# Optimization experiments

Measured on AMD Instinct MI355X. Metric: run time of the kernel, lower is better.

The kernel has to match this reference:

```python
import jax, jax.numpy as jnp
import numpy as np

B, L, E, H = 4, 4096, 1024, 16
D = E // H
SQRT_D = float(np.sqrt(D))


def _g(x):
    # torch: softplus(x, beta=5) ** 2
    sp = jax.nn.softplus(5.0 * x) / 5.0
    return sp * sp


def setup_inputs() -> dict:
    key = jax.random.key(0)
    ks = jax.random.split(key, 7)
    s = 1.0 / np.sqrt(E)
    x = jax.random.normal(ks[0], (B, L, E), jnp.float32)
    Wq = jax.random.normal(ks[1], (E, E), jnp.float32) * s
    bq = jax.random.normal(ks[2], (E,), jnp.float32) * s
    Wk = jax.random.normal(ks[3], (E, E), jnp.float32) * s
    bk = jax.random.normal(ks[4], (E,), jnp.float32) * s
    Wv = jax.random.normal(ks[5], (E, E), jnp.float32) * s
    bv = jax.random.normal(ks[6], (E,), jnp.float32) * s
    return {"x": x, "Wq": Wq, "bq": bq, "Wk": Wk, "bk": bk, "Wv": Wv, "bv": bv}


def _fast_linear_attn(q, k, v):
    # q,k,v: [B,S,H,D]
    Ls = q.shape[1]
    # RALA-style global-query rescaling of K
    q_global = q.mean(axis=1, keepdims=True) / SQRT_D          # [B,1,H,D]
    logits = jnp.einsum('bihd,blhd->bihl', q_global, k)        # [B,1,H,L]
    alpha = jax.nn.softmax(logits, axis=-1) * Ls               # [B,1,H,L]
    alpha = jnp.transpose(alpha[:, 0], (0, 2, 1))[..., None]   # [B,L,H,1]
    k = k * alpha
    gq, gk = _g(q), _g(k)
    gmq, gmk = _g(-q), _g(-k)
    # symmetric / antisymmetric KV accumulation: state [B,H,D,D]
    gk_v = jnp.einsum('bshd,bshv->bhdv', gk, v)
    gmk_v = jnp.einsum('bshd,bshv->bhdv', gmk, v)
    num = (jnp.einsum('bshd,bhdv->bshv', gq, gk_v)
           + jnp.einsum('bshd,bhdv->bshv', gmq, gmk_v))        # [B,S,H,D]
    den = (jnp.einsum('bshd,bhd->bsh', gq, gk.sum(axis=1))
           + jnp.einsum('bshd,bhd->bsh', gmq, gmk.sum(axis=1)))
    return num / (den[..., None] + 1e-6)


def reference(x, Wq, bq, Wk, bk, Wv, bv):
    q = (x @ Wq + bq).reshape(B, L, H, D)
    k = (x @ Wk + bk).reshape(B, L, H, D)
    v = (x @ Wv + bv).reshape(B, L, H, D)
    out = _fast_linear_attn(q, k, v)  # [B,L,H,D]
    return out.reshape(B, L, E)
```

## Files before the change

### kernel.cpp

```cpp
#include <hip/hip_runtime.h>
#include <hip/hip_bf16.h>
#include <math.h>

#define B_ 4
#define L_ 4096
#define E_ 1024
#define H_ 16
#define D_ 64
#define M_ (B_*L_)

typedef __attribute__((ext_vector_type(8))) short s8;
typedef __attribute__((ext_vector_type(4))) float f4;

__device__ __forceinline__ float gfun(float x) {
  float z = fminf(5.0f * x, 60.0f);
  float sp = 0.2f * __logf(1.0f + __expf(z));
  return sp * sp;
}

__device__ __forceinline__ unsigned short f2bf(float v) {
  __hip_bfloat16 h = __float2bfloat16(v);
  return *reinterpret_cast<unsigned short*>(&h);
}
__device__ __forceinline__ float bf2f(unsigned short u) {
  __hip_bfloat16 h = *reinterpret_cast<__hip_bfloat16*>(&u);
  return __bfloat162float(h);
}

__device__ __forceinline__ void gload16(const void* g, void* l) {
  __builtin_amdgcn_global_load_lds(
      (const __attribute__((address_space(1))) void*)g,
      (__attribute__((address_space(3))) void*)l, 16, 0, 0);
}

__global__ __launch_bounds__(256) void split_x(
    const float* __restrict__ x, unsigned short* __restrict__ Ah,
    float* __restrict__ xsum)
{
  int blk = blockIdx.x, t = threadIdx.x;
  int r0 = blk * 64, b = r0 >> 12;
  int c4 = t * 4;
  float4 cs = {0.f, 0.f, 0.f, 0.f};
  for (int r = 0; r < 64; ++r) {
    int row = r0 + r;
    float4 x4 = *(const float4*)(x + (size_t)row * E_ + c4);
    ushort4 hi, lo;
    unsigned short h;
    h = f2bf(x4.x); hi.x = h; lo.x = f2bf(x4.x - bf2f(h));
    h = f2bf(x4.y); hi.y = h; lo.y = f2bf(x4.y - bf2f(h));
    h = f2bf(x4.z); hi.z = h; lo.z = f2bf(x4.z - bf2f(h));
    h = f2bf(x4.w); hi.w = h; lo.w = f2bf(x4.w - bf2f(h));
    *(ushort4*)&Ah[(size_t)row * 2048 + c4]        = hi;
    *(ushort4*)&Ah[(size_t)row * 2048 + 1024 + c4] = lo;
    cs.x += x4.x; cs.y += x4.y; cs.z += x4.z; cs.w += x4.w;
  }
  atomicAdd(&xsum[b * E_ + c4 + 0], cs.x);
  atomicAdd(&xsum[b * E_ + c4 + 1], cs.y);
  atomicAdd(&xsum[b * E_ + c4 + 2], cs.z);
  atomicAdd(&xsum[b * E_ + c4 + 3], cs.w);
}

__global__ __launch_bounds__(256) void split_wT(
    const float* __restrict__ Wq, const float* __restrict__ Wk,
    const float* __restrict__ Wv, const float* __restrict__ bq,
    const float* __restrict__ xsum,
    unsigned short* __restrict__ Bt, float* __restrict__ qg)
{
  int z = blockIdx.z;
  const float* W = (z == 0) ? Wq : (z == 1) ? Wk : Wv;
  __shared__ float tile[32][33];
  int t = threadIdx.x;
  int tx = t & 31, ty = t >> 5;
  int k0 = blockIdx.x * 32, n0 = blockIdx.y * 32;
  #pragma unroll
  for (int i = 0; i < 4; ++i)
    tile[ty + i*8][tx] = W[(size_t)(k0 + ty + i*8) * 1024 + n0 + tx];
  __syncthreads();
  unsigned short* Bz = Bt + (size_t)z * 2097152;
  #pragma unroll
  for (int i = 0; i < 4; ++i) {
    int n = n0 + ty + i*8, kk = k0 + tx;
    float v = tile[tx][ty + i*8];
    unsigned short h = f2bf(v);
    Bz[(size_t)n * 2048 + kk]        = h;
    Bz[(size_t)n * 2048 + 1024 + kk] = f2bf(v - bf2f(h));
  }
  if (z == 0 && t < 128) {
    int n = t & 31, b = t >> 5;
    float dot = 0.f;
    #pragma unroll
    for (int kk = 0; kk < 32; ++kk)
      dot += xsum[b * E_ + k0 + kk] * tile[kk][n];
    float val = dot * (1.0f / (L_ * 8.0f));
    if (k0 == 0) val += bq[n0 + n] * 0.125f;
    atomicAdd(&qg[b * E_ + n0 + n], val);
  }
}

#define PRIO1() __builtin_amdgcn_s_setprio(1)
#define PRIO0() __builtin_amdgcn_s_setprio(0)
#define BARR() do { asm volatile("" ::: "memory"); \
                    __builtin_amdgcn_s_barrier(); \
                    asm volatile("" ::: "memory"); } while (0)
#define WAITL0() asm volatile("s_waitcnt lgkmcnt(0)" ::: "memory")
#define WAITV(n) asm volatile("s_waitcnt vmcnt(" n ")" ::: "memory")

#define STAGE_A(buf, kofs) do { \
  const unsigned short* g_ = gA + (kofs); \
  char* d_ = dA0 + (buf) * 32768; \
  gload16(g_,          d_); \
  gload16(g_ + 131072, d_ +  8192); \
  gload16(g_ + 262144, d_ + 16384); \
  gload16(g_ + 393216, d_ + 24576); \
} while (0)

#define STAGE_B(buf, kofs) do { \
  const unsigned short* g_ = gB + (kofs); \
  char* d_ = dB0 + (buf) * 32768; \
  gload16(g_,          d_); \
  gload16(g_ + 131072, d_ +  8192); \
  gload16(g_ + 262144, d_ + 16384); \
  gload16(g_ + 393216, d_ + 24576); \
} while (0)

#define LDA(buf, mh) do { \
  const char* p_ = shb + (buf) * 32768 + arow + (mh) * 8192; \
  _Pragma("unroll") \
  for (int ii = 0; ii < 4; ++ii) { \
    aF[ii][0] = *(const s8*)(p_ + ii * 2048 + c0); \
    aF[ii][1] = *(const s8*)(p_ + ii * 2048 + c1); \
  } \
} while (0)

#define LDB(buf, nh) do { \
  const char* p_ = shb + 65536 + (buf) * 32768 + brow + (nh) * 4096; \
  _Pragma("unroll") \
  for (int jj = 0; jj < 2; ++jj) { \
    bF[(nh)*2+jj][0] = *(const s8*)(p_ + jj * 2048 + c0); \
    bF[(nh)*2+jj][1] = *(const s8*)(p_ + jj * 2048 + c1); \
  } \
} while (0)

#define MFMAQ(mh, nh) do { \
  _Pragma("unroll") \
  for (int ii = 0; ii < 4; ++ii) \
    _Pragma("unroll") \
    for (int jj = 0; jj < 2; ++jj) { \
      acc[(mh)*4+ii][(nh)*2+jj] = __builtin_amdgcn_mfma_f32_16x16x32_bf16( \
          aF[ii][0], bF[(nh)*2+jj][0], acc[(mh)*4+ii][(nh)*2+jj], 0, 0, 0); \
      acc[(mh)*4+ii][(nh)*2+jj] = __builtin_amdgcn_mfma_f32_16x16x32_bf16( \
          aF[ii][1], bF[(nh)*2+jj][1], acc[(mh)*4+ii][(nh)*2+jj], 0, 0, 0); \
    } \
} while (0)

#define TILE2(buf, doStage, kB_, kA_, vmN) do { \
   \
  LDA(buf, 0); LDB(buf, 0); LDB(buf, 1); \
  WAITL0(); \
  PRIO1(); MFMAQ(0, 0); MFMAQ(0, 1); PRIO0(); \
   \
  LDA(buf, 1); \
  BARR(); \
  WAITL0(); \
  if (doStage) { STAGE_B(buf, kB_); STAGE_A(buf, kA_); } \
  PRIO1(); MFMAQ(1, 0); MFMAQ(1, 1); PRIO0(); \
  WAITV(vmN); \
  BARR(); \
} while (0)

__global__ __launch_bounds__(512, 2) void qkv_mfma(
    const unsigned short* __restrict__ Ah, const unsigned short* __restrict__ Bt,
    const float* __restrict__ bq, const float* __restrict__ bk,
    const float* __restrict__ bv, const float* __restrict__ qg,
    float* __restrict__ aexp, float* __restrict__ denom,
    float* __restrict__ qo, float* __restrict__ ko, float* __restrict__ vo)
{
  __shared__ unsigned short sh[65536];

  const int t  = threadIdx.x;
  const int li = blockIdx.x;
  const int xc = li & 7;
  const int idx = li >> 3;
  const int z   = idx >> 5;
  const int rem = idx & 31;
  const int bm = (xc * 8 + (rem >> 2)) * 256;
  const int bn = (rem & 3) * 256;

  const float* bias = (z == 0) ? bq : (z == 1) ? bk : bv;
  float* out = (z == 0) ? qo : (z == 1) ? ko : vo;
  const unsigned short* Bz = Bt + (size_t)z * 2097152;

  const int srow = t >> 3;
  const int scol = ((t & 7) ^ (srow & 7)) * 8;
  const unsigned short* gA = Ah + (size_t)(bm + srow) * 2048 + scol;
  const unsigned short* gB = Bz + (size_t)(bn + srow) * 2048 + scol;
  char* const shb = (char*)sh;
  char* const dA0 = shb +         t * 16;
  char* const dB0 = shb + 65536 + t * 16;

  const int lane = t & 63, wid = t >> 6;
  const int wm = wid >> 2, wn = wid & 3;
  const int fr = lane & 15, fq = lane >> 4;
  const int c0 = ((fq)     ^ (fr & 7)) * 16;
  const int c1 = ((fq + 4) ^ (fr & 7)) * 16;
  const int arow = (wm * 128 + fr) * 128;
  const int brow = (wn *  64 + fr) * 128;

  f4 acc[8][4] = {};
  s8 aF[4][2], bF[4][2];

  STAGE_B(0, 0);  STAGE_A(0, 0);
  STAGE_B(1, 64); STAGE_A(1, 64);
  WAITV("8");
  BARR();

  #pragma unroll 1
  for (int it = 0; it < 23; ++it) {
    const int t2 = 2 * it + 2, t3 = 2 * it + 3;
    const int kA2 = (t2 < 16) ? t2 * 64 : t2 * 64 - 1024;
    const int kB2 = (t2 < 32) ? t2 * 64 : t2 * 64 - 2048;
    const int kA3 = (t3 < 16) ? t3 * 64 : t3 * 64 - 1024;
    const int kB3 = (t3 < 32) ? t3 * 64 : t3 * 64 - 2048;
    TILE2(0, true, kB2, kA2, "8");
    TILE2(1, true, kB3, kA3, "8");
  }
  TILE2(0, false, 0, 0, "0");
  TILE2(1, false, 0, 0, "0");

  float bv4[4];
  #pragma unroll
  for (int j = 0; j < 4; ++j) bv4[j] = bias[bn + wn * 64 + j * 16 + fr];
  #pragma unroll
  for (int i = 0; i < 8; ++i) {
    const int mrow = bm + wm * 128 + i * 16 + fq * 4;
    #pragma unroll
    for (int j = 0; j < 4; ++j) {
      const int ncol = bn + wn * 64 + j * 16 + fr;
      #pragma unroll
      for (int r = 0; r < 4; ++r)
        out[(size_t)(mrow + r) * E_ + ncol] = acc[i][j][r] + bv4[j];
    }
  }

  if (z == 1) {
    const int b_ = bm >> 12;
    const int h  = (bn >> 6) + wn;
    const int bh = b_ * 16 + h;
    float qgv[4];
    #pragma unroll
    for (int j = 0; j < 4; ++j) qgv[j] = qg[bh * 64 + j * 16 + fr];
    float partial[8][4];
    #pragma unroll
    for (int i = 0; i < 8; ++i)
      #pragma unroll
      for (int r = 0; r < 4; ++r) {
        float p = 0.f;
        #pragma unroll
        for (int j = 0; j < 4; ++j)
          p += qgv[j] * (acc[i][j][r] + bv4[j]);
        p += __shfl_xor(p, 1);
        p += __shfl_xor(p, 2);
        p += __shfl_xor(p, 4);
        p += __shfl_xor(p, 8);
        partial[i][r] = p;
      }
    if (fr == 0) {
      const int lbase = (bm & 4095) + wm * 128 + fq * 4;
      float s = 0.f;
      #pragma unroll
      for (int i = 0; i < 8; ++i)
        #pragma unroll
        for (int r = 0; r < 4; ++r) {
          float e = __expf(partial[i][r]);
          aexp[(size_t)bh * 4096 + lbase + i * 16 + r] = e;
          s += e;
        }
      atomicAdd(&denom[bh], s);
    }
  }
}

__global__ __launch_bounds__(256) void state_part(
    const float* __restrict__ k, const float* __restrict__ v,
    const float* __restrict__ aexp, const float* __restrict__ denom,
    float* __restrict__ Spart, float* __restrict__ SMpart,
    float* __restrict__ kpart, float* __restrict__ kmpart)
{
  __shared__ unsigned short lds[24576];
  const int bh = blockIdx.x, b = bh >> 4, h = bh & 15;
  const int c = blockIdx.y;
  const float scale = (float)L_ / denom[bh];
  const int t = threadIdx.x;

  const int wid = t >> 6, lane = t & 63;
  const int s = wid >> 1, dh = wid & 1;
  const int fr = lane & 15, fq = lane >> 4;
  const int lp = t >> 3, dg8 = (t & 7) * 8;
  const int kd = t & 63, isM = (t >> 6) & 1;
  const int kx7 = kd & 7;
  const unsigned short* AT = lds + s * 8192;
  const unsigned short* VT = lds + 16384;

  f4 acc[2][4] = {};
  float ksr = 0.f;

  #pragma unroll 1
  for (int sc = 0; sc < 2; ++sc) {
    const int l0 = c * 128 + sc * 64 + 2 * lp;
    const size_t r0 = (size_t)(b * L_ + l0) * E_ + h * 64 + dg8;
    float4 kE0 = *(const float4*)(k + r0);
    float4 kE1 = *(const float4*)(k + r0 + 4);
    float4 kO0 = *(const float4*)(k + r0 + E_);
    float4 kO1 = *(const float4*)(k + r0 + E_ + 4);
    float4 vE0 = *(const float4*)(v + r0);
    float4 vE1 = *(const float4*)(v + r0 + 4);
    float4 vO0 = *(const float4*)(v + r0 + E_);
    float4 vO1 = *(const float4*)(v + r0 + E_ + 4);
    const float av0 = aexp[(size_t)bh * L_ + l0]     * scale;
    const float av1 = aexp[(size_t)bh * L_ + l0 + 1] * scale;
    const float ke[8] = {kE0.x,kE0.y,kE0.z,kE0.w,kE1.x,kE1.y,kE1.z,kE1.w};
    const float ko[8] = {kO0.x,kO0.y,kO0.z,kO0.w,kO1.x,kO1.y,kO1.z,kO1.w};
    const float ve[8] = {vE0.x,vE0.y,vE0.z,vE0.w,vE1.x,vE1.y,vE1.z,vE1.w};
    const float vo[8] = {vO0.x,vO0.y,vO0.z,vO0.w,vO1.x,vO1.y,vO1.z,vO1.w};
    if (sc) __syncthreads();
    const int usl = 2 * lp;
    #pragma unroll
    for (int j = 0; j < 8; ++j) {
      const int d = dg8 + j, x7 = d & 7;
      const int ph = d * 128 + (((usl >> 3)) ^ x7) * 8 + (usl & 7);
      const int pl = ph + 64;
      const float ge = gfun( ke[j] * av0), go = gfun( ko[j] * av1);
      const float me = gfun(-ke[j] * av0), mo = gfun(-ko[j] * av1);
      unsigned short eh, oh;
      eh = f2bf(ge); oh = f2bf(go);
      *(unsigned int*)&lds[ph] = (unsigned)eh | ((unsigned)oh << 16);
      eh = f2bf(ge - bf2f(eh)); oh = f2bf(go - bf2f(oh));
      *(unsigned int*)&lds[pl] = (unsigned)eh | ((unsigned)oh << 16);
      eh = f2bf(me); oh = f2bf(mo);
      *(unsigned int*)&lds[8192 + ph] = (unsigned)eh | ((unsigned)oh << 16);
      eh = f2bf(me - bf2f(eh)); oh = f2bf(mo - bf2f(oh));
      *(unsigned int*)&lds[8192 + pl] = (unsigned)eh | ((unsigned)oh << 16);
      eh = f2bf(ve[j]); oh = f2bf(vo[j]);
      *(unsigned int*)&lds[16384 + ph] = (unsigned)eh | ((unsigned)oh << 16);
      eh = f2bf(ve[j] - bf2f(eh)); oh = f2bf(vo[j] - bf2f(oh));
      *(unsigned int*)&lds[16384 + pl] = (unsigned)eh | ((unsigned)oh << 16);
    }
    __syncthreads();
    #pragma unroll
    for (int ks = 0; ks < 6; ++ks) {
      const int seg = ks >> 1, loc = ks & 1;
      const int ac = loc * 32 + fq * 8 + ((seg == 2) ? 64 : 0);
      const int bc = loc * 32 + fq * 8 + ((seg == 1) ? 64 : 0);
      s8 aF[2], bF[4];
      #pragma unroll
      for (int m = 0; m < 2; ++m) {
        const int row = dh * 32 + m * 16 + fr;
        aF[m] = *(const s8*)&AT[row * 128 + ((ac >> 3) ^ (row & 7)) * 8];
      }
      #pragma unroll
      for (int n = 0; n < 4; ++n) {
        const int row = n * 16 + fr;
        bF[n] = *(const s8*)&VT[row * 128 + ((bc >> 3) ^ (row & 7)) * 8];
      }
      #pragma unroll
      for (int m = 0; m < 2; ++m)
        #pragma unroll
        for (int n = 0; n < 4; ++n)
          acc[m][n] = __builtin_amdgcn_mfma_f32_16x16x32_bf16(
              aF[m], bF[n], acc[m][n], 0, 0, 0);
    }
    if (t < 128) {
      const unsigned short* R = lds + isM * 8192 + kd * 128;
      #pragma unroll
      for (int sl = 0; sl < 16; ++sl) {
        s8 w8 = *(const s8*)&R[(sl ^ kx7) * 8];
        #pragma unroll
        for (int e = 0; e < 8; ++e)
          ksr += bf2f((unsigned short)w8[e]);
      }
    }
  }

  float* Sp = (s == 0) ? Spart : SMpart;
  const size_t pb = ((size_t)(c * 64 + bh)) * 4096;
  #pragma unroll
  for (int m = 0; m < 2; ++m)
    #pragma unroll
    for (int n = 0; n < 4; ++n)
      #pragma unroll
      for (int r = 0; r < 4; ++r) {
        const int d  = dh * 32 + m * 16 + fq * 4 + r;
        const int vv = n * 16 + fr;
        Sp[pb + d * 64 + vv] = acc[m][n][r];
      }
  if (t < 128)
    (isM ? kmpart : kpart)[(c * 64 + bh) * 64 + kd] = ksr;
}

__global__ __launch_bounds__(256) void state_reduce(
    const float* __restrict__ Spart, const float* __restrict__ SMpart,
    const float* __restrict__ kpart, const float* __restrict__ kmpart,
    float* __restrict__ S, float* __restrict__ Sm,
    float* __restrict__ ksum, float* __restrict__ kmsum)
{
  int bh = blockIdx.x, seg = blockIdx.y, t = threadIdx.x;
  int idx = seg * 1024 + t * 4;
  float4 s = {0,0,0,0}, sm = {0,0,0,0};
  #pragma unroll
  for (int p = 0; p < 32; ++p) {
    float4 a = *(const float4*)&Spart [((size_t)(p*64 + bh))*4096 + idx];
    float4 c = *(const float4*)&SMpart[((size_t)(p*64 + bh))*4096 + idx];
    s.x += a.x; s.y += a.y; s.z += a.z; s.w += a.w;
    sm.x += c.x; sm.y += c.y; sm.z += c.z; sm.w += c.w;
  }
  *(float4*)&S [(size_t)bh*4096 + idx] = s;
  *(float4*)&Sm[(size_t)bh*4096 + idx] = sm;
  if (seg == 0 && t < 64) {
    float a = 0.f, c = 0.f;
    #pragma unroll
    for (int p = 0; p < 32; ++p) {
      a += kpart [(p*64 + bh)*64 + t];
      c += kmpart[(p*64 + bh)*64 + t];
    }
    ksum [bh*64 + t] = a;
    kmsum[bh*64 + t] = c;
  }
}

__global__ __launch_bounds__(128, 4) void out_kernel(
    const float* __restrict__ q,
    const float* __restrict__ S, const float* __restrict__ Sm,
    const float* __restrict__ ksum, const float* __restrict__ kmsum,
    float* __restrict__ out)
{
  int bh = blockIdx.x; int b = bh >> 4, h = bh & 15;
  int l0 = blockIdx.y * 64;
  __shared__ float Gq[64][64], Gm[64][64];
  int t = threadIdx.x;

  int lr = t >> 1, dq = (t & 1) * 32;
  const float4* qp = (const float4*)(q + (size_t)(b*L_ + l0 + lr)*E_ + h*64 + dq);
  #pragma unroll
  for (int j = 0; j < 8; ++j) {
    float4 qv = qp[j];
    float vals[4] = {qv.x, qv.y, qv.z, qv.w};
    #pragma unroll
    for (int jj = 0; jj < 4; ++jj) {
      int dd = dq + j*4 + jj;
      Gq[dd][lr] = gfun(vals[jj]);
      Gm[dd][lr] = gfun(-vals[jj]);
    }
  }
  __syncthreads();

  int tn = (t & 7) * 8, tm = (t >> 3) * 4;
  const float* Sp   = S  + (size_t)bh*4096;
  const float* Smp  = Sm + (size_t)bh*4096;
  const float* ksp  = ksum  + bh*64;
  const float* kmsp = kmsum + bh*64;
  float acc[4][8] = {};
  float den[4] = {};
  #pragma unroll 2
  for (int kk = 0; kk < 64; ++kk) {
    float4 ga = *(const float4*)&Gq[kk][tm];
    float4 ma = *(const float4*)&Gm[kk][tm];
    float4 s0 = *(const float4*)&Sp [kk*64 + tn];
    float4 s1 = *(const float4*)&Sp [kk*64 + tn + 4];
    float4 m0 = *(const float4*)&Smp[kk*64 + tn];
    float4 m1 = *(const float4*)&Smp[kk*64 + tn + 4];
    float ksv = ksp[kk], kmv = kmsp[kk];
    float gv[4] = {ga.x, ga.y, ga.z, ga.w};
    float mv[4] = {ma.x, ma.y, ma.z, ma.w};
    float sv[8] = {s0.x, s0.y, s0.z, s0.w, s1.x, s1.y, s1.z, s1.w};
    float smv[8] = {m0.x, m0.y, m0.z, m0.w, m1.x, m1.y, m1.z, m1.w};
    #pragma unroll
    for (int i = 0; i < 4; ++i) {
      #pragma unroll
      for (int j = 0; j < 8; ++j)
        acc[i][j] += gv[i]*sv[j] + mv[i]*smv[j];
      den[i] += gv[i]*ksv + mv[i]*kmv;
    }
  }

  #pragma unroll
  for (int i = 0; i < 4; ++i) {
    float r = 1.0f / (den[i] + 1e-6f);
    float4 o0, o1;
    o0.x = acc[i][0]*r; o0.y = acc[i][1]*r; o0.z = acc[i][2]*r; o0.w = acc[i][3]*r;
    o1.x = acc[i][4]*r; o1.y = acc[i][5]*r; o1.z = acc[i][6]*r; o1.w = acc[i][7]*r;
    size_t ro = (size_t)(b*L_ + l0 + tm + i)*E_ + h*64 + tn;
    *(float4*)(out + ro)     = o0;
    *(float4*)(out + ro + 4) = o1;
  }
}

extern "C" void kernel_launch(void* const* d_in, const int* in_sizes, int n_in,
                              void* d_out, int out_size, void* d_ws, size_t ws_size,
                              hipStream_t stream) {
  const float* x  = (const float*)d_in[0];
  const float* Wq = (const float*)d_in[1];
  const float* bq = (const float*)d_in[2];
  const float* Wk = (const float*)d_in[3];
  const float* bk = (const float*)d_in[4];
  const float* Wv = (const float*)d_in[5];
  const float* bv = (const float*)d_in[6];
  float* out = (float*)d_out;
  float* ws  = (float*)d_ws;

  float* q      = ws;
  float* k      = ws + 16777216;
  float* qg     = ws + 33554432;
  float* denom  = ws + 33558528;
  float* xsum   = ws + 33558592;
  float* S      = ws + 33562688;
  float* Sm     = ws + 33824832;
  float* ksum   = ws + 34086976;
  float* kmsum  = ws + 34091072;
  float* aexp   = ws + 34095168;
  unsigned short* Ah = (unsigned short*)(ws + 34357312);
  unsigned short* Bt = (unsigned short*)(ws + 51134528);
  float* Spart  = ws + 34357312;
  float* SMpart = ws + 42745920;
  float* kpart  = ws + 51134528;
  float* kmpart = ws + 51265600;
  float* v      = out;

  hipMemsetAsync(qg, 0, 8256 * sizeof(float), stream);

  split_x<<<256, 256, 0, stream>>>(x, Ah, xsum);
  split_wT<<<dim3(32, 32, 3), 256, 0, stream>>>(Wq, Wk, Wv, bq, xsum, Bt, qg);
  qkv_mfma<<<dim3(768), 512, 0, stream>>>(Ah, Bt, bq, bk, bv, qg,
                                          aexp, denom, q, k, v);
  state_part<<<dim3(B_*H_, 32), 256, 0, stream>>>(k, v, aexp, denom,
                                                  Spart, SMpart, kpart, kmpart);
  state_reduce<<<dim3(B_*H_, 4), 256, 0, stream>>>(Spart, SMpart, kpart, kmpart,
                                                   S, Sm, ksum, kmsum);
  out_kernel<<<dim3(B_*H_, 64), 128, 0, stream>>>(q, S, Sm, ksum, kmsum, out);
}
```

Before: 620.4 us.

## Compute output projection with bf16x3 MFMA using packed transposed state

The output kernel's scalar FP32 FMA loop over the 64x64 state is replaced with bf16 MFMA instructions, using a hi/lo split of both g(q) and the state to keep accuracy. The state reduction now writes a transposed, bf16-split packed buffer that also carries the key sums as an extra column, so the denominator falls out of the same MFMA. LDS tiles are XOR-swizzled and the state is loaded asynchronously. This trades extra MFMA work and precision-split overhead for removing the FP32 inner loop.

Result: faster. 544.4 us (-12.3%).

```diff
diff --git a/kernel.cpp b/kernel.cpp
--- a/kernel.cpp
+++ b/kernel.cpp
@@ -154,11 +154,9 @@
 } while (0)
 
 #define TILE2(buf, doStage, kB_, kA_, vmN) do { \
-   \
   LDA(buf, 0); LDB(buf, 0); LDB(buf, 1); \
   WAITL0(); \
   PRIO1(); MFMAQ(0, 0); MFMAQ(0, 1); PRIO0(); \
-   \
   LDA(buf, 1); \
   BARR(); \
   WAITL0(); \
@@ -400,11 +398,11 @@
 __global__ __launch_bounds__(256) void state_reduce(
     const float* __restrict__ Spart, const float* __restrict__ SMpart,
     const float* __restrict__ kpart, const float* __restrict__ kmpart,
-    float* __restrict__ S, float* __restrict__ Sm,
-    float* __restrict__ ksum, float* __restrict__ kmsum)
+    unsigned short* __restrict__ SBT)
 {
   int bh = blockIdx.x, seg = blockIdx.y, t = threadIdx.x;
   int idx = seg * 1024 + t * 4;
+  int d = idx >> 6, vv = idx & 63;
   float4 s = {0,0,0,0}, sm = {0,0,0,0};
   #pragma unroll
   for (int p = 0; p < 32; ++p) {
@@ -413,84 +411,132 @@
     s.x += a.x; s.y += a.y; s.z += a.z; s.w += a.w;
     sm.x += c.x; sm.y += c.y; sm.z += c.z; sm.w += c.w;
   }
-  *(float4*)&S [(size_t)bh*4096 + idx] = s;
-  *(float4*)&Sm[(size_t)bh*4096 + idx] = sm;
-  if (seg == 0 && t < 64) {
-    float a = 0.f, c = 0.f;
-    #pragma unroll
-    for (int p = 0; p < 32; ++p) {
-      a += kpart [(p*64 + bh)*64 + t];
-      c += kmpart[(p*64 + bh)*64 + t];
-    }
-    ksum [bh*64 + t] = a;
-    kmsum[bh*64 + t] = c;
-  }
-}
-
-__global__ __launch_bounds__(128, 4) void out_kernel(
-    const float* __restrict__ q,
-    const float* __restrict__ S, const float* __restrict__ Sm,
-    const float* __restrict__ ksum, const float* __restrict__ kmsum,
+  unsigned short* SB = SBT + (size_t)bh * 20480;
+  const float sa[4] = {s.x, s.y, s.z, s.w};
+  const float sb[4] = {sm.x, sm.y, sm.z, sm.w};
+  #pragma unroll
+  for (int j = 0; j < 4; ++j) {
+    unsigned short h1 = f2bf(sa[j]);
+    SB[(vv + j) * 256 + d]       = h1;
+    SB[(vv + j) * 256 + 64 + d]  = f2bf(sa[j] - bf2f(h1));
+    unsigned short h2 = f2bf(sb[j]);
+    SB[(vv + j) * 256 + 128 + d] = h2;
+    SB[(vv + j) * 256 + 192 + d] = f2bf(sb[j] - bf2f(h2));
+  }
+  if (seg == 0) {
+    if (t < 64) {
+      float a = 0.f, c = 0.f;
+      #pragma unroll
+      for (int p = 0; p < 32; ++p) {
+        a += kpart [(p*64 + bh)*64 + t];
+        c += kmpart[(p*64 + bh)*64 + t];
+      }
+      unsigned short h = f2bf(a);
+      SB[64*256 + t]       = h;
+      SB[64*256 + 64 + t]  = f2bf(a - bf2f(h));
+      h = f2bf(c);
+      SB[64*256 + 128 + t] = h;
+      SB[64*256 + 192 + t] = f2bf(c - bf2f(h));
+    }
+    for (int i = t; i < 15 * 256; i += 256)
+      SB[65*256 + i] = 0;
+  }
+}
+
+__global__ __launch_bounds__(256, 2) void out_kernel(
+    const float* __restrict__ q, const unsigned short* __restrict__ SBT,
     float* __restrict__ out)
 {
-  int bh = blockIdx.x; int b = bh >> 4, h = bh & 15;
-  int l0 = blockIdx.y * 64;
-  __shared__ float Gq[64][64], Gm[64][64];
-  int t = threadIdx.x;
-
-  int lr = t >> 1, dq = (t & 1) * 32;
-  const float4* qp = (const float4*)(q + (size_t)(b*L_ + l0 + lr)*E_ + h*64 + dq);
-  #pragma unroll
-  for (int j = 0; j < 8; ++j) {
-    float4 qv = qp[j];
-    float vals[4] = {qv.x, qv.y, qv.z, qv.w};
-    #pragma unroll
-    for (int jj = 0; jj < 4; ++jj) {
-      int dd = dq + j*4 + jj;
-      Gq[dd][lr] = gfun(vals[jj]);
-      Gm[dd][lr] = gfun(-vals[jj]);
-    }
-  }
+  __shared__ unsigned short lds[36864];
+  const int bh = blockIdx.x, b = bh >> 4, h = bh & 15;
+  const int l0 = blockIdx.y * 64;
+  const int t = threadIdx.x;
+  char* const shb = (char*)lds;
+
+  {
+    const unsigned short* SBg = SBT + (size_t)bh * 20480;
+    const int sl = t & 31, rb = t >> 5;
+    const unsigned short* src = SBg + rb * 256 + ((sl ^ (rb & 7)) * 8);
+    char* dst = shb + 32768 + t * 16;
+    #pragma unroll
+    for (int i = 0; i < 10; ++i)
+      gload16(src + i * 2048, dst + (size_t)i * 4096);
+  }
+
+  {
+    const int lr = t >> 2, dq = (t & 3) * 16;
+    const float* qrow = q + (size_t)(b * L_ + l0 + lr) * E_ + h * 64 + dq;
+    float qv[16];
+    #pragma unroll
+    for (int i = 0; i < 4; ++i) {
+      float4 x = *(const float4*)(qrow + i * 4);
+      qv[i*4+0] = x.x; qv[i*4+1] = x.y; qv[i*4+2] = x.z; qv[i*4+3] = x.w;
+    }
+    const int x7 = lr & 7;
+    #pragma unroll
+    for (int oct = 0; oct < 2; ++oct) {
+      const int sb = (dq >> 3) + oct;
+      s8 ghi, glo, mhi, mlo;
+      #pragma unroll
+      for (int j = 0; j < 8; ++j) {
+        float qx = qv[oct * 8 + j];
+        float g = gfun(qx);
+        unsigned short gh = f2bf(g);
+        ghi[j] = (short)gh;
+        glo[j] = (short)f2bf(g - bf2f(gh));
+        float m = gfun(-qx);
+        unsigned short mh = f2bf(m);
+        mhi[j] = (short)mh;
+        mlo[j] = (short)f2bf(m - bf2f(mh));
+      }
+      char* base = shb + lr * 512 + ((sb ^ x7) * 16);
+      *(s8*)(base)        = ghi;
+      *(s8*)(base + 128)  = glo;
+      *(s8*)(base + 256)  = mhi;
+      *(s8*)(base + 384)  = mlo;
+    }
+  }
+  WAITV("0");
   __syncthreads();
 
-  int tn = (t & 7) * 8, tm = (t >> 3) * 4;
-  const float* Sp   = S  + (size_t)bh*4096;
-  const float* Smp  = Sm + (size_t)bh*4096;
-  const float* ksp  = ksum  + bh*64;
-  const float* kmsp = kmsum + bh*64;
-  float acc[4][8] = {};
-  float den[4] = {};
-  #pragma unroll 2
-  for (int kk = 0; kk < 64; ++kk) {
-    float4 ga = *(const float4*)&Gq[kk][tm];
-    float4 ma = *(const float4*)&Gm[kk][tm];
-    float4 s0 = *(const float4*)&Sp [kk*64 + tn];
-    float4 s1 = *(const float4*)&Sp [kk*64 + tn + 4];
-    float4 m0 = *(const float4*)&Smp[kk*64 + tn];
-    float4 m1 = *(const float4*)&Smp[kk*64 + tn + 4];
-    float ksv = ksp[kk], kmv = kmsp[kk];
-    float gv[4] = {ga.x, ga.y, ga.z, ga.w};
-    float mv[4] = {ma.x, ma.y, ma.z, ma.w};
-    float sv[8] = {s0.x, s0.y, s0.z, s0.w, s1.x, s1.y, s1.z, s1.w};
-    float smv[8] = {m0.x, m0.y, m0.z, m0.w, m1.x, m1.y, m1.z, m1.w};
-    #pragma unroll
-    for (int i = 0; i < 4; ++i) {
-      #pragma unroll
-      for (int j = 0; j < 8; ++j)
-        acc[i][j] += gv[i]*sv[j] + mv[i]*smv[j];
-      den[i] += gv[i]*ksv + mv[i]*kmv;
-    }
-  }
-
-  #pragma unroll
-  for (int i = 0; i < 4; ++i) {
-    float r = 1.0f / (den[i] + 1e-6f);
-    float4 o0, o1;
-    o0.x = acc[i][0]*r; o0.y = acc[i][1]*r; o0.z = acc[i][2]*r; o0.w = acc[i][3]*r;
-    o1.x = acc[i][4]*r; o1.y = acc[i][5]*r; o1.z = acc[i][6]*r; o1.w = acc[i][7]*r;
-    size_t ro = (size_t)(b*L_ + l0 + tm + i)*E_ + h*64 + tn;
-    *(float4*)(out + ro)     = o0;
-    *(float4*)(out + ro + 4) = o1;
+  const int wid = t >> 6, lane = t & 63;
+  const int fr = lane & 15, fq = lane >> 4;
+  const int arow = wid * 16 + fr;
+  const int ax7 = fr & 7;
+  f4 acc[5] = {{0.f,0.f,0.f,0.f},{0.f,0.f,0.f,0.f},{0.f,0.f,0.f,0.f},
+               {0.f,0.f,0.f,0.f},{0.f,0.f,0.f,0.f}};
+  #pragma unroll
+  for (int ks = 0; ks < 12; ++ks) {
+    const int st = ks / 6, rm = ks % 6, sg = rm >> 1, lc = rm & 1;
+    const int acol = st * 128 + ((sg == 2) ? 64 : 0) + lc * 32 + fq * 8;
+    const int bcol = st * 128 + ((sg == 1) ? 64 : 0) + lc * 32 + fq * 8;
+    s8 aF = *(const s8*)(shb + arow * 512 + (((acol >> 3) ^ ax7) * 16));
+    s8 bF[5];
+    #pragma unroll
+    for (int n = 0; n < 5; ++n) {
+      const int brow = n * 16 + fr;
+      bF[n] = *(const s8*)(shb + 32768 + brow * 512 +
+                           (((bcol >> 3) ^ (brow & 7)) * 16));
+    }
+    #pragma unroll
+    for (int n = 0; n < 5; ++n)
+      acc[n] = __builtin_amdgcn_mfma_f32_16x16x32_bf16(aF, bF[n], acc[n], 0, 0, 0);
+  }
+
+  float rden[4];
+  #pragma unroll
+  for (int r = 0; r < 4; ++r) {
+    float dsum = __shfl(acc[4][r], lane & 48);
+    rden[r] = 1.0f / (dsum + 1e-6f);
+  }
+  #pragma unroll
+  for (int n = 0; n < 4; ++n) {
+    const int col = h * 64 + n * 16 + fr;
+    #pragma unroll
+    for (int r = 0; r < 4; ++r) {
+      const size_t row = (size_t)(b * L_ + l0 + wid * 16 + fq * 4 + r);
+      out[row * E_ + col] = acc[n][r] * rden[r];
+    }
   }
 }
 
@@ -512,10 +558,7 @@
   float* qg     = ws + 33554432;
   float* denom  = ws + 33558528;
   float* xsum   = ws + 33558592;
-  float* S      = ws + 33562688;
-  float* Sm     = ws + 33824832;
-  float* ksum   = ws + 34086976;
-  float* kmsum  = ws + 34091072;
+  unsigned short* SBT = (unsigned short*)(ws + 33562688);
   float* aexp   = ws + 34095168;
   unsigned short* Ah = (unsigned short*)(ws + 34357312);
   unsigned short* Bt = (unsigned short*)(ws + 51134528);
@@ -534,6 +577,6 @@
   state_part<<<dim3(B_*H_, 32), 256, 0, stream>>>(k, v, aexp, denom,
                                                   Spart, SMpart, kpart, kmpart);
   state_reduce<<<dim3(B_*H_, 4), 256, 0, stream>>>(Spart, SMpart, kpart, kmpart,
-                                                   S, Sm, ksum, kmsum);
-  out_kernel<<<dim3(B_*H_, 64), 128, 0, stream>>>(q, S, Sm, ksum, kmsum, out);
-}
+                                                   SBT);
+  out_kernel<<<dim3(B_*H_, 64), 256, 0, stream>>>(q, SBT, out);
+}
```
